# Optimization experiments

Measured on AMD Instinct MI355X. Metric: run time of the kernel, lower is better.

Reference implementation:

```python
import jax, jax.numpy as jnp
from jax import lax
import numpy as np

B, T, D_IN = 4, 1024, 8
D_MODEL, N_LAYERS, HORIZON, D_OUT = 512, 2, 24, 8
D_STATE, D_CONV, EXPAND = 64, 4, 2
D_INNER = EXPAND * D_MODEL
DT_RANK = -(-D_MODEL // 16)  # ceil(d_model/16) = 32
LN_EPS = 1e-5


def setup_inputs() -> dict:
    key = jax.random.key(0)
    ks = iter(jax.random.split(key, 24))
    rn = lambda shape, s: jax.random.normal(next(ks), shape, jnp.float32) * s
    A_log = jnp.tile(jnp.log(jnp.arange(1, D_STATE + 1, dtype=jnp.float32)), (N_LAYERS, D_INNER, 1))
    return {
        "x": rn((B, T, D_IN), 1.0),
        "W_in": rn((D_IN, D_MODEL), 0.3), "b_in": jnp.zeros((D_MODEL,), jnp.float32),
        "W_xz": rn((N_LAYERS, D_MODEL, 2 * D_INNER), 0.04),
        "conv_w": rn((N_LAYERS, D_INNER, D_CONV), 0.3), "conv_b": jnp.zeros((N_LAYERS, D_INNER), jnp.float32),
        "W_xproj": rn((N_LAYERS, D_INNER, DT_RANK + 2 * D_STATE), 0.03),
        "W_dt": rn((N_LAYERS, DT_RANK, D_INNER), 0.1), "b_dt": rn((N_LAYERS, D_INNER), 0.1) - 4.0,
        "A_log": A_log, "D_skip": jnp.ones((N_LAYERS, D_INNER), jnp.float32),
        "W_out": rn((N_LAYERS, D_INNER, D_MODEL), 0.03),
        "ln_g": jnp.ones((D_MODEL,), jnp.float32), "ln_b": jnp.zeros((D_MODEL,), jnp.float32),
        "W_h1": rn((D_MODEL, D_MODEL), 0.04), "b_h1": jnp.zeros((D_MODEL,), jnp.float32),
        "W_h2": rn((D_MODEL, HORIZON * D_OUT), 0.04), "b_h2": jnp.zeros((HORIZON * D_OUT,), jnp.float32),
    }


def mamba_block(h, Wxz, cw, cb, Wxp, Wdt, bdt, Alog, Dsk, Wout):
    # h: [B,T,d_model] -> [B,T,d_model]  (mamba-ssm Mamba block, no residual)
    xz = h @ Wxz                                   # [B,T,2*d_inner]
    xb, z = jnp.split(xz, 2, axis=-1)
    # depthwise causal conv over time
    xc = jnp.transpose(xb, (0, 2, 1))              # [B,d_inner,T]
    xc = lax.conv_general_dilated(xc, cw[:, None, :], (1,), [(D_CONV - 1, 0)],
                                  feature_group_count=D_INNER)
    xc = jax.nn.silu(xc + cb[None, :, None])
    xc = jnp.transpose(xc, (0, 2, 1))              # [B,T,d_inner]
    # input-dependent dt, B, C
    xdb = xc @ Wxp                                 # [B,T,dt_rank+2*d_state]
    dt_r = xdb[..., :DT_RANK]
    Bc = xdb[..., DT_RANK:DT_RANK + D_STATE]
    Cc = xdb[..., DT_RANK + D_STATE:]
    dt = jax.nn.softplus(dt_r @ Wdt + bdt)         # [B,T,d_inner]
    A = -jnp.exp(Alog)                             # [d_inner,d_state]

    def step(hst, ins):
        dt_t, B_t, C_t, x_t = ins                  # [B,d_inner],[B,N],[B,N],[B,d_inner]
        dA = jnp.exp(dt_t[..., None] * A)          # [B,d_inner,N]
        hst = dA * hst + dt_t[..., None] * B_t[:, None, :] * x_t[..., None]
        y = jnp.einsum('bdn,bn->bd', hst, C_t)
        return hst, y

    h0 = jnp.zeros((h.shape[0], D_INNER, D_STATE), h.dtype)
    xs = (jnp.transpose(dt, (1, 0, 2)), jnp.transpose(Bc, (1, 0, 2)),
          jnp.transpose(Cc, (1, 0, 2)), jnp.transpose(xc, (1, 0, 2)))
    _, ys = lax.scan(step, h0, xs)                 # ys: [T,B,d_inner]
    y = jnp.transpose(ys, (1, 0, 2)) + Dsk * xc
    y = y * jax.nn.silu(z)
    return y @ Wout


def reference(x, W_in, b_in, W_xz, conv_w, conv_b, W_xproj, W_dt, b_dt, A_log, D_skip,
              W_out, ln_g, ln_b, W_h1, b_h1, W_h2, b_h2):
    h = x @ W_in + b_in                            # [B,T,d_model]
    for i in range(N_LAYERS):
        h = mamba_block(h, W_xz[i], conv_w[i], conv_b[i], W_xproj[i], W_dt[i],
                        b_dt[i], A_log[i], D_skip[i], W_out[i])
    mu = jnp.mean(h, axis=-1, keepdims=True)
    var = jnp.mean(jnp.square(h - mu), axis=-1, keepdims=True)
    h = (h - mu) * lax.rsqrt(var + LN_EPS) * ln_g + ln_b
    last = h[:, -1, :]                             # [B,d_model]
    hid = jax.nn.gelu(last @ W_h1 + b_h1, approximate=False)
    yhat = hid @ W_h2 + b_h2                       # [B,horizon*d_out]
    return yhat.reshape(x.shape[0], HORIZON, D_OUT)
```

## Files before the change

### kernel.cpp

```cpp
#include <hip/hip_runtime.h>
#include <hip/hip_bf16.h>

static constexpr int kB      = 4;
static constexpr int kT      = 1024;
static constexpr int kDIN    = 8;
static constexpr int kDMODEL = 512;
static constexpr int kHOR    = 24;
static constexpr int kDOUT   = 8;
static constexpr int kDSTATE = 64;
static constexpr int kDINNER = 1024;
static constexpr int kDTRANK = 32;
static constexpr int kXPROJ  = 160;
static constexpr int kXPAD   = 256;
static constexpr int kBT     = kB * kT;
static constexpr int kNLAYER = 2;

typedef __bf16 bf16x8 __attribute__((ext_vector_type(8)));
typedef float  f32x4  __attribute__((ext_vector_type(4)));

__device__ __forceinline__ float silu_f(float x)     { return x / (1.f + __expf(-x)); }
__device__ __forceinline__ float softplus_f(float x) { return (x > 20.f) ? x : log1pf(__expf(x)); }
__device__ __forceinline__ float gelu_f(float x)     { return 0.5f * x * (1.f + erff(x * 0.70710678118654752f)); }

__device__ __forceinline__ void gld_lds16(const void* g, void* l) {
    __builtin_amdgcn_global_load_lds(
        (const __attribute__((address_space(1))) unsigned int*)g,
        (__attribute__((address_space(3))) unsigned int*)l, 16, 0, 0);
}

template<int CTRL>
__device__ __forceinline__ float dpp_mov(float v) {
    return __int_as_float(__builtin_amdgcn_update_dpp(
        0, __float_as_int(v), CTRL, 0xf, 0xf, false));
}

__global__ __launch_bounds__(256) void wtrans_all_kernel(
    const float* __restrict__ Wxz, const float* __restrict__ Wxp,
    const float* __restrict__ Wdt, const float* __restrict__ Wout,
    __hip_bfloat16* __restrict__ oxz, __hip_bfloat16* __restrict__ oxp,
    __hip_bfloat16* __restrict__ odt, __hip_bfloat16* __restrict__ oout)
{
    __shared__ float tile[32][33];
    const int bid = blockIdx.x;
    const int tid = threadIdx.x;

    const float* in; __hip_bfloat16* out;
    int K, N, Kpad, TX, loc;
    if (bid < 2048) {
        int l = bid >> 10; loc = bid & 1023;
        in = Wxz + (size_t)l * 512 * 2048; out = oxz + (size_t)l * 2048 * 512;
        K = 512; N = 2048; Kpad = 512; TX = 64;
    } else if (bid < 2368) {
        int r = bid - 2048; int l = r / 160; loc = r % 160;
        in = Wxp + (size_t)l * 1024 * 160; out = oxp + (size_t)l * 256 * 1024;
        K = 1024; N = 160; Kpad = 1024; TX = 5;
    } else if (bid < 2496) {
        int r = bid - 2368; int l = r >> 6; loc = r & 63;
        in = Wdt + (size_t)l * 32 * 1024; out = odt + (size_t)l * 1024 * 64;
        K = 32; N = 1024; Kpad = 64; TX = 32;
    } else {
        int r = bid - 2496; int l = r >> 9; loc = r & 511;
        in = Wout + (size_t)l * 1024 * 512; out = oout + (size_t)l * 512 * 1024;
        K = 1024; N = 512; Kpad = 1024; TX = 16;
    }
    const int n0 = (loc % TX) * 32;
    const int k0 = (loc / TX) * 32;

#pragma unroll
    for (int p = 0; p < 4; ++p) {
        int idx = p * 256 + tid;
        int ki = idx >> 5, ni = idx & 31;
        float v = 0.f;
        if (k0 + ki < K && n0 + ni < N) v = in[(size_t)(k0 + ki) * N + n0 + ni];
        tile[ki][ni] = v;
    }
    __syncthreads();
#pragma unroll
    for (int p = 0; p < 4; ++p) {
        int idx = p * 256 + tid;
        int ni = idx >> 5, ki = idx & 31;
        if (n0 + ni < N)
            out[(size_t)(n0 + ni) * Kpad + k0 + ki] = __float2bfloat16(tile[ki][ni]);
    }
}

__global__ __launch_bounds__(256) void wfold_kernel(
    const float* __restrict__ Win, const float* __restrict__ bin,
    const float* __restrict__ Wxz0, float* __restrict__ wf)
{
    __shared__ float sred[3][64][9];
    const int t    = threadIdx.x & 63;
    const int part = threadIdx.x >> 6;
    const int col  = blockIdx.x * 64 + t;

    float acc[9];
#pragma unroll
    for (int r = 0; r < 9; ++r) acc[r] = 0.f;

    const int k0 = part * 128;
#pragma unroll 4
    for (int k = k0; k < k0 + 128; ++k) {
        float wv = Wxz0[(size_t)k * 2048 + col];
#pragma unroll
        for (int r = 0; r < 8; ++r)
            acc[r] = fmaf(Win[r * kDMODEL + k], wv, acc[r]);
        acc[8] = fmaf(bin[k], wv, acc[8]);
    }
    if (part > 0) {
#pragma unroll
        for (int r = 0; r < 9; ++r) sred[part - 1][t][r] = acc[r];
    }
    __syncthreads();
    if (part == 0) {
#pragma unroll
        for (int r = 0; r < 9; ++r)
            wf[(size_t)col * 12 + r] =
                acc[r] + sred[0][t][r] + sred[1][t][r] + sred[2][t][r];
    }
}

__global__ __launch_bounds__(256) void xz0_kernel(
    const float* __restrict__ x, const float* __restrict__ wf,
    __hip_bfloat16* __restrict__ xb, __hip_bfloat16* __restrict__ z)
{
    int idx = blockIdx.x * 256 + threadIdx.x;
    int m  = idx >> 9;
    int n4 = (idx & 511) * 4;
    const float* xr = x + m * kDIN;
    float xv[8];
#pragma unroll
    for (int r = 0; r < 8; ++r) xv[r] = xr[r];

    float acc[4];
#pragma unroll
    for (int c = 0; c < 4; ++c) {
        const float* w = wf + (size_t)(n4 + c) * 12;
        float a = w[8];
#pragma unroll
        for (int r = 0; r < 8; ++r) a = fmaf(xv[r], w[r], a);
        acc[c] = a;
    }
    __bf16 o4[4];
    if (n4 < kDINNER) {
#pragma unroll
        for (int c = 0; c < 4; ++c) o4[c] = (__bf16)acc[c];
        *reinterpret_cast<ushort4*>(xb + (size_t)m * kDINNER + n4) =
            *reinterpret_cast<ushort4*>(o4);
    } else {
#pragma unroll
        for (int c = 0; c < 4; ++c) o4[c] = (__bf16)silu_f(acc[c]);
        *reinterpret_cast<ushort4*>(z + (size_t)m * kDINNER + n4 - kDINNER) =
            *reinterpret_cast<ushort4*>(o4);
    }
}

template<int MODE, int BM, int BN>
__global__ __launch_bounds__(256) void mfma_gemm_bt(
    const __hip_bfloat16* __restrict__ A, int lda,
    const __hip_bfloat16* __restrict__ BT, int ldb,
    const float* __restrict__ bias,
    float* __restrict__ C, int ldc,
    void* __restrict__ C2,
    int K)
{
    constexpr int WN  = (BM == 128 && BN == 64) ? 1 : 2;
    constexpr int WM  = 4 / WN;
    constexpr int WTM = BM / WM;
    constexpr int WTN = BN / WN;
    constexpr int MI  = WTM / 16;
    constexpr int NJ  = WTN / 16;

    __shared__ __align__(16) __hip_bfloat16 sA[BM][64];
    __shared__ __align__(16) __hip_bfloat16 sB[BN][64];

    const int tid  = threadIdx.x;
    const int lane = tid & 63;
    const int w    = tid >> 6;
    const int m0   = blockIdx.y * BM;
    const int n0   = blockIdx.x * BN;
    const int wm   = (WN == 1) ? w : (w >> 1);
    const int wn   = (WN == 1) ? 0 : (w & 1);

    f32x4 acc[MI][NJ] = {};

    const int lrow = lane & 15;
    const int lk   = (lane >> 4) << 3;

    const int grow = tid >> 3;
    const int gcol = (tid & 7) * 8;
    char* ldsA = (char*)&sA[0][0] + w * 1024;
    char* ldsB = (char*)&sB[0][0] + w * 1024;

    for (int k0 = 0; k0 < K; k0 += 64) {
        __syncthreads();
#pragma unroll
        for (int p = 0; p < BM / 32; ++p)
            gld_lds16(A + (size_t)(m0 + grow + p * 32) * lda + k0 + gcol, ldsA + p * 4096);
#pragma unroll
        for (int p = 0; p < BN / 32; ++p)
            gld_lds16(BT + (size_t)(n0 + grow + p * 32) * ldb + k0 + gcol, ldsB + p * 4096);
        __syncthreads();
#pragma unroll
        for (int ks = 0; ks < 2; ++ks) {
            bf16x8 af[MI], bfr[NJ];
#pragma unroll
            for (int i = 0; i < MI; ++i)
                af[i] = *reinterpret_cast<const bf16x8*>(&sA[wm * WTM + i * 16 + lrow][ks * 32 + lk]);
#pragma unroll
            for (int j = 0; j < NJ; ++j)
                bfr[j] = *reinterpret_cast<const bf16x8*>(&sB[wn * WTN + j * 16 + lrow][ks * 32 + lk]);
#pragma unroll
            for (int i = 0; i < MI; ++i)
#pragma unroll
                for (int j = 0; j < NJ; ++j)
                    acc[i][j] = __builtin_amdgcn_mfma_f32_16x16x32_bf16(af[i], bfr[j], acc[i][j], 0, 0, 0);
        }
    }

    const int crow = (lane >> 4) * 4;
    const int ccol = lane & 15;
#pragma unroll
    for (int i = 0; i < MI; ++i) {
#pragma unroll
        for (int j = 0; j < NJ; ++j) {
#pragma unroll
            for (int r = 0; r < 4; ++r) {
                int row = m0 + wm * WTM + i * 16 + crow + r;
                int col = n0 + wn * WTN + j * 16 + ccol;
                float v = acc[i][j][r];
                if (MODE == 1) {
                    C[(size_t)row * ldc + col] = v;
                    ((__hip_bfloat16*)C2)[(size_t)row * ldc + col] = __float2bfloat16(v);
                } else if (MODE == 2) {
                    C[(size_t)row * ldc + col] = softplus_f(v + bias[col]);
                } else if (MODE == 4) {
                    if (col < kDINNER)
                        ((__hip_bfloat16*)C)[(size_t)row * ldc + col] = __float2bfloat16(v);
                    else
                        ((__hip_bfloat16*)C2)[(size_t)row * ldc + (col - kDINNER)] =
                            __float2bfloat16(silu_f(v));
                } else {
                    if (col < kDTRANK)
                        ((__hip_bfloat16*)C2)[(size_t)row * kXPAD + col] = __float2bfloat16(v);
                    else if (col < kDTRANK + kDSTATE)
                        C[(size_t)(row >> 1) * 256 + (col - kDTRANK) * 4 + (row & 1) * 2] = v;
                    else if (col < kXPROJ)
                        C[(size_t)(row >> 1) * 256 + (col - kDTRANK - kDSTATE) * 4 + (row & 1) * 2 + 1] = v;
                }
            }
        }
    }
}

__global__ __launch_bounds__(256) void conv_silu_kernel(
    const __hip_bfloat16* __restrict__ xb,
    const float* __restrict__ cw, const float* __restrict__ cb,
    __hip_bfloat16* __restrict__ xc)
{
    int idx = blockIdx.x * 256 + threadIdx.x;
    int dg  = (idx & 127) * 8;
    int bt  = idx >> 7;
    int t   = bt & (kT - 1);

    float4 wv[8];
#pragma unroll
    for (int k = 0; k < 8; ++k)
        wv[k] = *reinterpret_cast<const float4*>(cw + (dg + k) * 4);

    float acc[8];
#pragma unroll
    for (int k = 0; k < 8; ++k) acc[k] = cb[dg + k];

    const __hip_bfloat16* base = xb + (size_t)bt * kDINNER + dg;
    {
        bf16x8 v = *reinterpret_cast<const bf16x8*>(base);
#pragma unroll
        for (int k = 0; k < 8; ++k) acc[k] = fmaf((float)v[k], wv[k].w, acc[k]);
    }
    if (t >= 1) {
        bf16x8 v = *reinterpret_cast<const bf16x8*>(base - kDINNER);
#pragma unroll
        for (int k = 0; k < 8; ++k) acc[k] = fmaf((float)v[k], wv[k].z, acc[k]);
    }
    if (t >= 2) {
        bf16x8 v = *reinterpret_cast<const bf16x8*>(base - 2 * kDINNER);
#pragma unroll
        for (int k = 0; k < 8; ++k) acc[k] = fmaf((float)v[k], wv[k].y, acc[k]);
    }
    if (t >= 3) {
        bf16x8 v = *reinterpret_cast<const bf16x8*>(base - 3 * kDINNER);
#pragma unroll
        for (int k = 0; k < 8; ++k) acc[k] = fmaf((float)v[k], wv[k].x, acc[k]);
    }
    bf16x8 o;
#pragma unroll
    for (int k = 0; k < 8; ++k) o[k] = (__bf16)silu_f(acc[k]);
    *reinterpret_cast<bf16x8*>(xc + (size_t)bt * kDINNER + dg) = o;
}

__global__ __launch_bounds__(256, 4) void scan_kernel(
    const float* __restrict__ dt,
    const float* __restrict__ xdbi,
    const __hip_bfloat16* __restrict__ xc,
    const __hip_bfloat16* __restrict__ zs,
    const float* __restrict__ Alog,
    const float* __restrict__ Dsk,
    __hip_bfloat16* __restrict__ yg)
{
    __shared__ __align__(16) float sBC[2][16][64][4];
    __shared__ __align__(16) float sDT[2][16][4][4];

    const int tid  = threadIdx.x;
    const int lane = tid & 63;
    const int w    = tid >> 6;
    const int bb = blockIdx.x;
    const int b  = (bb & 7) >> 1;
    const int d0 = ((bb >> 3) + (bb & 1) * 128) * 4;
    const int d  = d0 + w;

    const float a2  = -__expf(Alog[d * kDSTATE + lane]) * 1.44269504f;
    const float dsk = Dsk[d];
    const size_t rowbase  = (size_t)b * kT;
    const size_t pairbase = (size_t)b * (kT / 2);
    float s = 0.f;

    auto stageBC = [&](int c, int buf) {
        const float* src = xdbi + (pairbase + c * 16 + 4 * w) * 256 + lane * 4;
#pragma unroll
        for (int p = 0; p < 4; ++p)
            gld_lds16(src + p * 256, &sBC[buf][4 * w + p][0][0]);
    };
    const int lp = tid >> 3, lw = (tid >> 1) & 3, lst = tid & 1;
    auto loadDT = [&](int c, float& odt, float& odx) {
        if (tid < 128) {
            size_t g = (rowbase + c * 32 + lp * 2 + lst) * kDINNER + d0 + lw;
            odt = dt[g];
            odx = odt * (float)((const __bf16*)xc)[g];
        }
    };
    auto writeDT = [&](int buf, float vdt, float vdx) {
        if (tid < 128) {
            sDT[buf][lp][lw][lst * 2]     = vdt;
            sDT[buf][lp][lw][lst * 2 + 1] = vdx;
        }
    };
    auto loadEP = [&](int c, float& oxv, float& ozv) {
        size_t g = (rowbase + c * 32 + (lane & 31)) * kDINNER + d;
        oxv = (float)((const __bf16*)xc)[g];
        ozv = (float)((const __bf16*)zs)[g];
    };

    float pdt = 0.f, pdx = 0.f, exv = 0.f, ezv = 0.f;
    stageBC(0, 0);
    loadDT(0, pdt, pdx);
    loadEP(0, exv, ezv);
    writeDT(0, pdt, pdx);
    __syncthreads();

    for (int c = 0; c < kT / 32; ++c) {
        const int buf = c & 1;
        float ndt = 0.f, ndx = 0.f, nxv = 0.f, nzv = 0.f;
        const bool more = (c + 1 < kT / 32);
        if (more) {
            stageBC(c + 1, buf ^ 1);
            loadDT(c + 1, ndt, ndx);
            loadEP(c + 1, nxv, nzv);
        }

        __builtin_amdgcn_s_setprio(1);
        float yv[32];
#pragma unroll
        for (int p = 0; p < 16; ++p) {
            float4 bc = *reinterpret_cast<const float4*>(&sBC[buf][p][lane][0]);
            float4 dd = *reinterpret_cast<const float4*>(&sDT[buf][p][w][0]);
            float dA0 = exp2f(dd.x * a2);
            s = fmaf(dA0, s, dd.y * bc.x);
            yv[2 * p] = s * bc.y;
            float dA1 = exp2f(dd.z * a2);
            s = fmaf(dA1, s, dd.w * bc.z);
            yv[2 * p + 1] = s * bc.w;
        }

#pragma unroll
        for (int m = 0; m < 16; ++m) {
            float av = yv[2 * m], bv = yv[2 * m + 1];
            float cv = (lane & 1) ? bv : av;
            float dv = (lane & 1) ? av : bv;
            yv[m] = cv + dpp_mov<0xB1>(dv);
        }
#pragma unroll
        for (int m = 0; m < 8; ++m) {
            float av = yv[2 * m], bv = yv[2 * m + 1];
            float cv = (lane & 2) ? bv : av;
            float dv = (lane & 2) ? av : bv;
            yv[m] = cv + dpp_mov<0x4E>(dv);
        }
#pragma unroll
        for (int j = 2; j < 5; ++j) {
            const int S = 1 << j;
#pragma unroll
            for (int m = 0; m < (32 >> (j + 1)); ++m) {
                float av = yv[2 * m], bv = yv[2 * m + 1];
                float cv = (lane & S) ? bv : av;
                float dv = (lane & S) ? av : bv;
                yv[m] = cv + __shfl_xor(dv, S, 64);
            }
        }
        float y = yv[0];
        y += __shfl_xor(y, 32, 64);
        __builtin_amdgcn_s_setprio(0);

        float yo = fmaf(dsk, exv, y) * ezv;
        if (lane < 32) {
            size_t g = (rowbase + c * 32 + lane) * kDINNER + d;
            yg[g] = __float2bfloat16(yo);
        }
        if (more) writeDT(buf ^ 1, ndt, ndx);
        __syncthreads();
        exv = nxv; ezv = nzv;
    }
}

__global__ __launch_bounds__(256) void ln_head_kernel(
    const float* __restrict__ h,
    const float* __restrict__ g, const float* __restrict__ be,
    const float* __restrict__ W1, const float* __restrict__ b1,
    const float* __restrict__ W2, const float* __restrict__ b2,
    float* __restrict__ out)
{
    __shared__ float sln[512];
    __shared__ float shid[512];
    __shared__ float sbuf[8];
    const int b = blockIdx.x, tid = threadIdx.x;
    const float* row = h + (size_t)(b * kT + (kT - 1)) * kDMODEL;

    float v0 = row[tid], v1 = row[tid + 256];
    float s = v0 + v1;
    float q = v0 * v0 + v1 * v1;
#pragma unroll
    for (int m = 32; m >= 1; m >>= 1) {
        s += __shfl_xor(s, m, 64);
        q += __shfl_xor(q, m, 64);
    }
    int wid = tid >> 6;
    if ((tid & 63) == 0) { sbuf[wid] = s; sbuf[4 + wid] = q; }
    __syncthreads();
    if (tid == 0) {
        float S = 0.f, Q = 0.f;
        for (int i = 0; i < 4; ++i) { S += sbuf[i]; Q += sbuf[4 + i]; }
        sbuf[0] = S; sbuf[4] = Q;
    }
    __syncthreads();
    float mean = sbuf[0] * (1.f / kDMODEL);
    float var  = sbuf[4] * (1.f / kDMODEL) - mean * mean;
    float inv  = rsqrtf(var + 1e-5f);
    sln[tid]       = (v0 - mean) * inv * g[tid]       + be[tid];
    sln[tid + 256] = (v1 - mean) * inv * g[tid + 256] + be[tid + 256];
    __syncthreads();

    float a0 = b1[tid], a1 = b1[tid + 256];
#pragma unroll 8
    for (int k = 0; k < kDMODEL; ++k) {
        float lv = sln[k];
        a0 = fmaf(lv, W1[(size_t)k * kDMODEL + tid],       a0);
        a1 = fmaf(lv, W1[(size_t)k * kDMODEL + tid + 256], a1);
    }
    shid[tid]       = gelu_f(a0);
    shid[tid + 256] = gelu_f(a1);
    __syncthreads();

    if (tid < kHOR * kDOUT) {
        float acc = b2[tid];
#pragma unroll 8
        for (int k = 0; k < kDMODEL; ++k)
            acc = fmaf(shid[k], W2[(size_t)k * (kHOR * kDOUT) + tid], acc);
        out[b * (kHOR * kDOUT) + tid] = acc;
    }
}

extern "C" void kernel_launch(void* const* d_in, const int* in_sizes, int n_in,
                              void* d_out, int out_size, void* d_ws, size_t ws_size,
                              hipStream_t stream)
{
    const float* x      = (const float*)d_in[0];
    const float* W_in   = (const float*)d_in[1];
    const float* b_in   = (const float*)d_in[2];
    const float* W_xz   = (const float*)d_in[3];
    const float* conv_w = (const float*)d_in[4];
    const float* conv_b = (const float*)d_in[5];
    const float* W_xp   = (const float*)d_in[6];
    const float* W_dt   = (const float*)d_in[7];
    const float* b_dt   = (const float*)d_in[8];
    const float* A_log  = (const float*)d_in[9];
    const float* D_skip = (const float*)d_in[10];
    const float* W_out  = (const float*)d_in[11];
    const float* ln_g   = (const float*)d_in[12];
    const float* ln_b   = (const float*)d_in[13];
    const float* W_h1   = (const float*)d_in[14];
    const float* b_h1   = (const float*)d_in[15];
    const float* W_h2   = (const float*)d_in[16];
    const float* b_h2   = (const float*)d_in[17];
    float* out = (float*)d_out;

    char* p = (char*)d_ws;
    auto alloc = [&](size_t bytes) { char* q = p; p += (bytes + 255) & ~(size_t)255; return q; };
    float*          h       = (float*)         alloc((size_t)kBT * kDMODEL * 4);
    __hip_bfloat16* h_bf    = (__hip_bfloat16*)alloc((size_t)kBT * kDMODEL * 2);
    __hip_bfloat16* xb_bf   = (__hip_bfloat16*)alloc((size_t)kBT * kDINNER * 2);
    __hip_bfloat16* z_bf    = (__hip_bfloat16*)alloc((size_t)kBT * kDINNER * 2);
    __hip_bfloat16* xc_bf   = (__hip_bfloat16*)alloc((size_t)kBT * kDINNER * 2);
    float*          xdbi    = (float*)         alloc((size_t)(kBT / 2) * 256 * 4);
    __hip_bfloat16* xdb_bf  = (__hip_bfloat16*)alloc((size_t)kBT * kXPAD * 2);
    float*          dtb     = (float*)         alloc((size_t)kBT * kDINNER * 4);
    __hip_bfloat16* ys_bf   = (__hip_bfloat16*)alloc((size_t)kBT * kDINNER * 2);
    __hip_bfloat16* wxz_bt  = (__hip_bfloat16*)alloc((size_t)2 * 2048 * 512 * 2);
    __hip_bfloat16* wxp_bt  = (__hip_bfloat16*)alloc((size_t)2 * 256 * 1024 * 2);
    __hip_bfloat16* wdt_bt  = (__hip_bfloat16*)alloc((size_t)2 * 1024 * 64 * 2);
    __hip_bfloat16* wout_bt = (__hip_bfloat16*)alloc((size_t)2 * 512 * 1024 * 2);
    float*          wfold   = (float*)         alloc((size_t)2048 * 12 * 4);

    wtrans_all_kernel<<<3520, 256, 0, stream>>>(
        W_xz, W_xp, W_dt, W_out, wxz_bt, wxp_bt, wdt_bt, wout_bt);
    wfold_kernel<<<32, 256, 0, stream>>>(W_in, b_in, W_xz, wfold);

    for (int l = 0; l < kNLAYER; ++l) {
        const float* cw_l  = conv_w + (size_t)l * kDINNER * 4;
        const float* cb_l  = conv_b + (size_t)l * kDINNER;
        const float* bdt_l = b_dt   + (size_t)l * kDINNER;
        const float* Al_l  = A_log  + (size_t)l * kDINNER * kDSTATE;
        const float* Dsk_l = D_skip + (size_t)l * kDINNER;
        const __hip_bfloat16* wxz_l  = wxz_bt  + (size_t)l * 2048 * 512;
        const __hip_bfloat16* wxp_l  = wxp_bt  + (size_t)l * 256 * 1024;
        const __hip_bfloat16* wdt_l  = wdt_bt  + (size_t)l * 1024 * 64;
        const __hip_bfloat16* wout_l = wout_bt + (size_t)l * 512 * 1024;

        if (l == 0) {
            xz0_kernel<<<(kBT * 512) / 256, 256, 0, stream>>>(x, wfold, xb_bf, z_bf);
        } else {
            mfma_gemm_bt<4, 128, 64><<<dim3(32, 32), 256, 0, stream>>>(
                h_bf, kDMODEL, wxz_l, 512, nullptr, (float*)xb_bf, kDINNER, z_bf, kDMODEL);
        }
        conv_silu_kernel<<<(kBT * 128) / 256, 256, 0, stream>>>(xb_bf, cw_l, cb_l, xc_bf);
        mfma_gemm_bt<5, 64, 64><<<dim3(3, 64), 256, 0, stream>>>(
            xc_bf, kDINNER, wxp_l, 1024, nullptr, xdbi, 0, xdb_bf, kDINNER);
        mfma_gemm_bt<2, 64, 64><<<dim3(16, 64), 256, 0, stream>>>(
            xdb_bf, kXPAD, wdt_l, 64, bdt_l, dtb, kDINNER, nullptr, 64);
        scan_kernel<<<kB * kDINNER / 4, 256, 0, stream>>>(
            dtb, xdbi, xc_bf, z_bf, Al_l, Dsk_l, ys_bf);
        mfma_gemm_bt<1, 64, 64><<<dim3(8, 64), 256, 0, stream>>>(
            ys_bf, kDINNER, wout_l, 1024, nullptr, h, kDMODEL, h_bf, kDINNER);
    }

    ln_head_kernel<<<kB, 256, 0, stream>>>(h, ln_g, ln_b, W_h1, b_h1, W_h2, b_h2, out);
}
```

Measured before the change: 477.2 us.

## Fuse layer-0 input projection with causal conv and software-pipeline scan reduction

For layer 0, the folded input projection is recomputed for the three previous timesteps inside the kernel, and the depthwise causal conv plus SiLU are applied there, so the separate conv kernel launch and the xb round trip are dropped. In the scan kernel, the butterfly reduction of the previous chunk is interleaved with the recurrence of the current chunk, using two yv register arrays. Global addresses now advance incrementally through pointers. The cost is fourfold redundant projection arithmetic in layer 0 and higher register pressure in the scan.

```diff
diff --git a/kernel.cpp b/kernel.cpp
--- a/kernel.cpp
+++ b/kernel.cpp
@@ -119,37 +119,70 @@
     }
 }
 
-__global__ __launch_bounds__(256) void xz0_kernel(
+__global__ __launch_bounds__(256) void xz0_conv_kernel(
     const float* __restrict__ x, const float* __restrict__ wf,
-    __hip_bfloat16* __restrict__ xb, __hip_bfloat16* __restrict__ z)
-{
-    int idx = blockIdx.x * 256 + threadIdx.x;
-    int m  = idx >> 9;
-    int n4 = (idx & 511) * 4;
-    const float* xr = x + m * kDIN;
-    float xv[8];
-#pragma unroll
-    for (int r = 0; r < 8; ++r) xv[r] = xr[r];
-
-    float acc[4];
+    const float* __restrict__ cw, const float* __restrict__ cb,
+    __hip_bfloat16* __restrict__ xcv, __hip_bfloat16* __restrict__ z)
+{
+    const int bid  = blockIdx.x;
+    const int m    = bid >> 1;
+    const int half = bid & 1;
+    const int t    = m & (kT - 1);
+    const int n4   = threadIdx.x * 4 + half * kDINNER;
+
+    float wreg[4][9];
 #pragma unroll
     for (int c = 0; c < 4; ++c) {
-        const float* w = wf + (size_t)(n4 + c) * 12;
-        float a = w[8];
-#pragma unroll
-        for (int r = 0; r < 8; ++r) a = fmaf(xv[r], w[r], a);
-        acc[c] = a;
-    }
-    __bf16 o4[4];
-    if (n4 < kDINNER) {
-#pragma unroll
-        for (int c = 0; c < 4; ++c) o4[c] = (__bf16)acc[c];
-        *reinterpret_cast<ushort4*>(xb + (size_t)m * kDINNER + n4) =
+        const float* wc = wf + (size_t)(n4 + c) * 12;
+#pragma unroll
+        for (int r = 0; r < 9; ++r) wreg[c][r] = wc[r];
+    }
+
+    if (half == 1) {
+        const float* xr = x + (size_t)m * kDIN;
+        float xv[8];
+#pragma unroll
+        for (int r = 0; r < 8; ++r) xv[r] = xr[r];
+        __bf16 o4[4];
+#pragma unroll
+        for (int c = 0; c < 4; ++c) {
+            float a = wreg[c][8];
+#pragma unroll
+            for (int r = 0; r < 8; ++r) a = fmaf(xv[r], wreg[c][r], a);
+            o4[c] = (__bf16)silu_f(a);
+        }
+        *reinterpret_cast<ushort4*>(z + (size_t)m * kDINNER + (n4 - kDINNER)) =
             *reinterpret_cast<ushort4*>(o4);
     } else {
+        float acc[4];
+        float4 cwv[4];
+#pragma unroll
+        for (int c = 0; c < 4; ++c) {
+            acc[c] = cb[n4 + c];
+            cwv[c] = *reinterpret_cast<const float4*>(cw + (n4 + c) * 4);
+        }
+#pragma unroll
+        for (int sh = 0; sh < 4; ++sh) {
+            if (t >= sh) {
+                const float* xr = x + (size_t)(m - sh) * kDIN;
+                float xv[8];
+#pragma unroll
+                for (int r = 0; r < 8; ++r) xv[r] = xr[r];
+#pragma unroll
+                for (int c = 0; c < 4; ++c) {
+                    float a = wreg[c][8];
+#pragma unroll
+                    for (int r = 0; r < 8; ++r) a = fmaf(xv[r], wreg[c][r], a);
+                    float wk = (sh == 0) ? cwv[c].w : (sh == 1) ? cwv[c].z
+                             : (sh == 2) ? cwv[c].y : cwv[c].x;
+                    acc[c] = fmaf(a, wk, acc[c]);
+                }
+            }
+        }
+        __bf16 o4[4];
 #pragma unroll
         for (int c = 0; c < 4; ++c) o4[c] = (__bf16)silu_f(acc[c]);
-        *reinterpret_cast<ushort4*>(z + (size_t)m * kDINNER + n4 - kDINNER) =
+        *reinterpret_cast<ushort4*>(xcv + (size_t)m * kDINNER + n4) =
             *reinterpret_cast<ushort4*>(o4);
     }
 }
@@ -324,51 +357,37 @@
     const size_t pairbase = (size_t)b * (kT / 2);
     float s = 0.f;
 
-    auto stageBC = [&](int c, int buf) {
-        const float* src = xdbi + (pairbase + c * 16 + 4 * w) * 256 + lane * 4;
+    const float* bcP = xdbi + (pairbase + 4 * w) * 256 + lane * 4;
+    const int lp = tid >> 3, lw = (tid >> 1) & 3, lst = tid & 1;
+    const float*  dtP  = dt + (rowbase + lp * 2 + lst) * kDINNER + d0 + lw;
+    const __bf16* xcDP = (const __bf16*)xc + (rowbase + lp * 2 + lst) * kDINNER + d0 + lw;
+    const __bf16* xcEP = (const __bf16*)xc + (rowbase + (lane & 31)) * kDINNER + d;
+    const __bf16* zsEP = (const __bf16*)zs + (rowbase + (lane & 31)) * kDINNER + d;
+    __hip_bfloat16* ygP = yg + (rowbase + (lane & 31)) * kDINNER + d;
+
+    float pdt = 0.f, pdx = 0.f;
+
+    auto stageBC = [&](int buf) {
 #pragma unroll
         for (int p = 0; p < 4; ++p)
-            gld_lds16(src + p * 256, &sBC[buf][4 * w + p][0][0]);
+            gld_lds16(bcP + p * 256, &sBC[buf][4 * w + p][0][0]);
+        bcP += 16 * 256;
     };
-    const int lp = tid >> 3, lw = (tid >> 1) & 3, lst = tid & 1;
-    auto loadDT = [&](int c, float& odt, float& odx) {
+    auto loadDT = [&]() {
         if (tid < 128) {
-            size_t g = (rowbase + c * 32 + lp * 2 + lst) * kDINNER + d0 + lw;
-            odt = dt[g];
-            odx = odt * (float)((const __bf16*)xc)[g];
+            pdt = *dtP;
+            pdx = pdt * (float)*xcDP;
+            dtP  += 32 * kDINNER;
+            xcDP += 32 * kDINNER;
         }
     };
-    auto writeDT = [&](int buf, float vdt, float vdx) {
+    auto writeDT = [&](int buf) {
         if (tid < 128) {
-            sDT[buf][lp][lw][lst * 2]     = vdt;
-            sDT[buf][lp][lw][lst * 2 + 1] = vdx;
+            sDT[buf][lp][lw][lst * 2]     = pdt;
+            sDT[buf][lp][lw][lst * 2 + 1] = pdx;
         }
     };
-    auto loadEP = [&](int c, float& oxv, float& ozv) {
-        size_t g = (rowbase + c * 32 + (lane & 31)) * kDINNER + d;
-        oxv = (float)((const __bf16*)xc)[g];
-        ozv = (float)((const __bf16*)zs)[g];
-    };
-
-    float pdt = 0.f, pdx = 0.f, exv = 0.f, ezv = 0.f;
-    stageBC(0, 0);
-    loadDT(0, pdt, pdx);
-    loadEP(0, exv, ezv);
-    writeDT(0, pdt, pdx);
-    __syncthreads();
-
-    for (int c = 0; c < kT / 32; ++c) {
-        const int buf = c & 1;
-        float ndt = 0.f, ndx = 0.f, nxv = 0.f, nzv = 0.f;
-        const bool more = (c + 1 < kT / 32);
-        if (more) {
-            stageBC(c + 1, buf ^ 1);
-            loadDT(c + 1, ndt, ndx);
-            loadEP(c + 1, nxv, nzv);
-        }
-
-        __builtin_amdgcn_s_setprio(1);
-        float yv[32];
+    auto recur = [&](int buf, float (&yv)[32]) {
 #pragma unroll
         for (int p = 0; p < 16; ++p) {
             float4 bc = *reinterpret_cast<const float4*>(&sBC[buf][p][lane][0]);
@@ -380,7 +399,8 @@
             s = fmaf(dA1, s, dd.w * bc.z);
             yv[2 * p + 1] = s * bc.w;
         }
-
+    };
+    auto tree = [&](float (&yv)[32]) -> float {
 #pragma unroll
         for (int m = 0; m < 16; ++m) {
             float av = yv[2 * m], bv = yv[2 * m + 1];
@@ -408,16 +428,51 @@
         }
         float y = yv[0];
         y += __shfl_xor(y, 32, 64);
+        return y;
+    };
+    auto body = [&](int c, float (&cur)[32], float (&prev)[32]) {
+        const bool more = (c + 1 < kT / 32);
+        if (more) { stageBC((c + 1) & 1); loadDT(); }
+        float exv = (float)*xcEP;
+        float ezv = (float)*zsEP;
+        __builtin_amdgcn_s_setprio(1);
+        recur(c & 1, cur);
+        float y = tree(prev);
         __builtin_amdgcn_s_setprio(0);
-
         float yo = fmaf(dsk, exv, y) * ezv;
-        if (lane < 32) {
-            size_t g = (rowbase + c * 32 + lane) * kDINNER + d;
-            yg[g] = __float2bfloat16(yo);
-        }
-        if (more) writeDT(buf ^ 1, ndt, ndx);
+        if (lane < 32) *ygP = __float2bfloat16(yo);
+        xcEP += 32 * kDINNER;
+        zsEP += 32 * kDINNER;
+        ygP  += 32 * kDINNER;
+        if (more) writeDT((c + 1) & 1);
         __syncthreads();
-        exv = nxv; ezv = nzv;
+    };
+
+    float yvA[32], yvB[32];
+
+    stageBC(0);
+    loadDT();
+    writeDT(0);
+    __syncthreads();
+
+    stageBC(1);
+    loadDT();
+    recur(0, yvA);
+    writeDT(1);
+    __syncthreads();
+
+    for (int cc = 1; cc < 31; cc += 2) {
+        body(cc,     yvB, yvA);
+        body(cc + 1, yvA, yvB);
+    }
+    body(31, yvB, yvA);
+
+    {
+        float exv = (float)*xcEP;
+        float ezv = (float)*zsEP;
+        float y = tree(yvB);
+        float yo = fmaf(dsk, exv, y) * ezv;
+        if (lane < 32) *ygP = __float2bfloat16(yo);
     }
 }
 
@@ -535,12 +590,13 @@
         const __hip_bfloat16* wout_l = wout_bt + (size_t)l * 512 * 1024;
 
         if (l == 0) {
-            xz0_kernel<<<(kBT * 512) / 256, 256, 0, stream>>>(x, wfold, xb_bf, z_bf);
+            xz0_conv_kernel<<<kBT * 2, 256, 0, stream>>>(
+                x, wfold, cw_l, cb_l, xc_bf, z_bf);
         } else {
             mfma_gemm_bt<4, 128, 64><<<dim3(32, 32), 256, 0, stream>>>(
                 h_bf, kDMODEL, wxz_l, 512, nullptr, (float*)xb_bf, kDINNER, z_bf, kDMODEL);
-        }
-        conv_silu_kernel<<<(kBT * 128) / 256, 256, 0, stream>>>(xb_bf, cw_l, cb_l, xc_bf);
+            conv_silu_kernel<<<(kBT * 128) / 256, 256, 0, stream>>>(xb_bf, cw_l, cb_l, xc_bf);
+        }
         mfma_gemm_bt<5, 64, 64><<<dim3(3, 64), 256, 0, stream>>>(
             xc_bf, kDINNER, wxp_l, 1024, nullptr, xdbi, 0, xdb_bf, kDINNER);
         mfma_gemm_bt<2, 64, 64><<<dim3(16, 64), 256, 0, stream>>>(
```

Result: slower. 1.048 ms (+119.7%).
